# Kernel optimization log

Hardware: AMD Instinct MI355X
Metric: run time of the kernel (lower is better)

## Reference

```python
import jax, jax.numpy as jnp
import numpy as np

CAR_DIM = 8
ESC_MAX_AGENT = 32
HID = 256
ACTION_DIM = 30
NUM_STATES = 64
BATCH = 8192
ENC_OUT = 1 + CAR_DIM * ESC_MAX_AGENT          # 257
Q_IN = 1 + CAR_DIM + CAR_DIM * ESC_MAX_AGENT   # 265


def setup_inputs() -> dict:
    key = jax.random.key(0)
    ks = jax.random.split(key, 9)
    s = jax.random.normal(ks[0], (BATCH, CAR_DIM + NUM_STATES * CAR_DIM), dtype=jnp.float32)
    def lin(k, fan_in, fan_out):
        bound = 1.0 / np.sqrt(fan_in)
        kw, kb = jax.random.split(k)
        W = jax.random.uniform(kw, (fan_in, fan_out), jnp.float32, -bound, bound)
        b = jax.random.uniform(kb, (fan_out,), jnp.float32, -bound, bound)
        return W, b
    W1, b1 = lin(ks[1], CAR_DIM, HID)
    W2, b2 = lin(ks[2], HID, ENC_OUT)
    Qw1, Qb1 = lin(ks[3], Q_IN, HID)
    Qw2, Qb2 = lin(ks[4], HID, ACTION_DIM)
    return {"s": s, "W1": W1, "b1": b1, "W2": W2, "b2": b2,
            "Qw1": Qw1, "Qb1": Qb1, "Qw2": Qw2, "Qb2": Qb2}


def reference(s, W1, b1, W2, b2, Qw1, Qb1, Qw2, Qb2):
    B = s.shape[0]
    self_states = s[:, :CAR_DIM]                                   # [B, C]
    surr = s[:, CAR_DIM:].reshape(B, -1, CAR_DIM)                  # [B, N, C]
    # sentinel agents: any coordinate exactly == -1 is skipped
    valid = ~jnp.any(surr == -1.0, axis=-1)                        # [B, N] bool
    h = jax.nn.relu(jnp.einsum('bnc,ch->bnh', surr, W1) + b1)      # [B, N, HID]
    enc = jax.nn.relu(jnp.einsum('bnh,he->bne', h, W2) + b2)       # [B, N, ENC_OUT]
    sum_outputs = jnp.sum(enc * valid[:, :, None].astype(enc.dtype), axis=1)  # [B, ENC_OUT]
    x = jnp.concatenate([self_states, sum_outputs], axis=1)        # [B, Q_IN]
    q = jax.nn.relu(x @ Qw1 + Qb1) @ Qw2 + Qb2                     # [B, ACTION_DIM]
    return q
```

## Files before the change

kernel.cpp:

```cpp
#include <hip/hip_runtime.h>

#define CAR 8
#define SROW 520
#define HID 256
#define EOUT 257
#define XPAD 288
#define ADIM 30

typedef __attribute__((ext_vector_type(8))) short sh8;
typedef __attribute__((ext_vector_type(4))) float f32x4;

__device__ __forceinline__ short f2bf(float f) {
  unsigned u = __builtin_bit_cast(unsigned, f);
  u += 0x7fffu + ((u >> 16) & 1u);
  return (short)(u >> 16);
}
__device__ __forceinline__ unsigned f2bf2(float a, float b) {
  unsigned ua = __builtin_bit_cast(unsigned, a);
  ua += 0x7fffu + ((ua >> 16) & 1u);
  unsigned ub = __builtin_bit_cast(unsigned, b);
  ub += 0x7fffu + ((ub >> 16) & 1u);
  return __builtin_amdgcn_perm(ub, ua, 0x07060302);
}
__device__ __forceinline__ unsigned pkt(float a, float b) {
  return __builtin_amdgcn_perm(__builtin_bit_cast(unsigned, b),
                               __builtin_bit_cast(unsigned, a), 0x07060302);
}

__global__ void k_prep(const float* __restrict__ W1, const float* __restrict__ b1,
                       const float* __restrict__ W2,
                       const float* __restrict__ Qw1, const float* __restrict__ Qw2,
                       short* __restrict__ w1f, short* __restrict__ w2f,
                       short* __restrict__ w3f, short* __restrict__ wq2f) {
  int idx = blockIdx.x * 256 + threadIdx.x;
  if (idx < 8192) {
    int mt = idx >> 9, r = idx & 511, lane = r >> 3, j = r & 7;
    int quad = lane >> 4, m = lane & 15;
    int hid = mt * 16 + m;
    float v = (quad == 0) ? W1[j * HID + hid]
            : (quad == 1 && j == 0) ? b1[hid] : 0.0f;
    w1f[idx] = f2bf(v);
    return;
  }
  int i2 = idx - 8192;
  if (i2 < 69632) {
    int ks = i2 / 8704, r = i2 % 8704;
    int nt = r >> 9, r2 = r & 511, lane = r2 >> 3, j = r2 & 7;
    int quad = lane >> 4, m = lane & 15;
    int k = ks * 32 + quad * 8 + j, n = nt * 16 + m;
    float v = (n < EOUT) ? W2[k * EOUT + n] : 0.0f;
    w2f[i2] = f2bf(v);
    return;
  }
  int i3 = i2 - 69632;
  if (i3 < 73728) {
    int ks = i3 >> 13, r = i3 & 8191;
    int nt = r >> 9, r2 = r & 511, lane = r2 >> 3, j = r2 & 7;
    int quad = lane >> 4, m = lane & 15;
    int k = ks * 32 + quad * 8 + j, n = nt * 16 + m;
    float v = (k < 265) ? Qw1[k * HID + n] : 0.0f;
    w3f[i3] = f2bf(v);
    return;
  }
  int i4 = i3 - 73728;
  if (i4 < 8192) {
    int ks = i4 >> 10, r = i4 & 1023;
    int nt = r >> 9, r2 = r & 511, lane = r2 >> 3, j = r2 & 7;
    int quad = lane >> 4, m = lane & 15;
    int k = ks * 32 + quad * 8 + j, n = nt * 16 + m;
    float v = (n < ADIM) ? Qw2[k * ADIM + n] : 0.0f;
    wq2f[i4] = f2bf(v);
  }
}

__global__ __launch_bounds__(512, 4)
void k_enc(const float* __restrict__ s, const short* __restrict__ w1f,
           const short* __restrict__ w2f, const float* __restrict__ b2,
           float* __restrict__ so288, int B) {
  __shared__ __align__(16) short hlds[2][16384];
  __shared__ float ninvp[8];
  __shared__ float t16[8][16];

  const int tid = threadIdx.x;
  const int w = tid >> 6, lane = tid & 63;
  const int q = lane >> 4, m = lane & 15;
  const int we = w >> 2, g = w & 3;
  const size_t bg0 = 2 * (size_t)blockIdx.x;
  size_t bg = bg0 + we; if (bg >= (size_t)B) bg = B - 1;

  const float* srow0 = s + bg * SROW + CAR;
  int4 pk = {0, 0, 0, 0};
  bool inv = false;
  if (lane < 16) {
    const float* sr = srow0 + (g * 16 + lane) * CAR;
    float4 f0 = ((const float4*)sr)[0], f1 = ((const float4*)sr)[1];
    inv = (f0.x == -1.f) | (f0.y == -1.f) | (f0.z == -1.f) | (f0.w == -1.f) |
          (f1.x == -1.f) | (f1.y == -1.f) | (f1.z == -1.f) | (f1.w == -1.f);
    if (!inv) {
      pk.x = (int)f2bf2(f0.x, f0.y); pk.y = (int)f2bf2(f0.z, f0.w);
      pk.z = (int)f2bf2(f1.x, f1.y); pk.w = (int)f2bf2(f1.z, f1.w);
    }
  }
  const float vflag = inv ? 0.f : 1.f;
  unsigned long long bal = __ballot(inv);
  if (lane == 0) ninvp[w] = (float)__popcll(bal);

  if (w == 1 || w == 2) {
    size_t rr = bg0 + (w - 1); if (rr >= (size_t)B) rr = B - 1;
    if (lane < CAR)       so288[rr * XPAD + lane] = s[rr * SROW + lane];
    else if (lane < 16)   so288[rr * XPAD + 280 + (lane - 8)] = 0.f;
  }

  int4 p0;
  p0.x = __shfl(pk.x, m, 64); p0.y = __shfl(pk.y, m, 64);
  p0.z = __shfl(pk.z, m, 64); p0.w = __shfl(pk.w, m, 64);
  const float vv0 = __shfl(vflag, m, 64);
  if (q == 1) {
    p0.x = (vv0 != 0.f) ? 0x3f80 : 0; p0.y = p0.z = p0.w = 0;
  } else if (q >= 2) {
    p0.x = p0.y = p0.z = p0.w = 0;
  }
  sh8 bs = __builtin_bit_cast(sh8, p0);

#pragma unroll 4
  for (int mt = 0; mt < 16; ++mt) {
    sh8 af = *(const sh8*)(w1f + (mt * 64 + lane) * 8);
    f32x4 z = {0.f, 0.f, 0.f, 0.f};
    f32x4 c0 = __builtin_amdgcn_mfma_f32_16x16x32_bf16(af, bs, z, 0, 0, 0);
    const int hidb = mt * 16 + q * 4;
    const int ks = hidb >> 5, qB = (hidb >> 3) & 3, js = hidb & 7;
    uint2 k0;
    k0.x = pkt(fmaxf(c0[0], 0.f), fmaxf(c0[1], 0.f));
    k0.y = pkt(fmaxf(c0[2], 0.f), fmaxf(c0[3], 0.f));
    *(uint2*)(&hlds[we][((g * 8 + ks) * 64 + qB * 16 + m) * 8 + js]) = k0;
  }
  __syncthreads();

  const int t0 = 2 * w;
  const float bi0  = b2[t0 * 16 + m];
  const float bi1  = b2[t0 * 16 + 16 + m];
  const float bi16 = (m == 0) ? b2[256] : 0.f;
  f32x4 acc[4][2][2];
  f32x4 acc16 = {bi16, bi16, bi16, bi16};
#pragma unroll
  for (int mtA = 0; mtA < 4; ++mtA)
#pragma unroll
    for (int e = 0; e < 2; ++e) {
      f32x4 c0 = {bi0, bi0, bi0, bi0};
      f32x4 c1 = {bi1, bi1, bi1, bi1};
      acc[mtA][0][e] = c0;
      acc[mtA][1][e] = c1;
    }
#pragma unroll
  for (int ks = 0; ks < 8; ++ks) {
    sh8 B0  = *(const sh8*)(w2f + ((ks * 17 + t0)     * 64 + lane) * 8);
    sh8 B1  = *(const sh8*)(w2f + ((ks * 17 + t0 + 1) * 64 + lane) * 8);
    sh8 B16 = *(const sh8*)(w2f + ((ks * 17 + 16)     * 64 + lane) * 8);
#pragma unroll
    for (int e = 0; e < 2; ++e) {
      sh8 A0 = *(const sh8*)(&hlds[e][(0 * 8 + ks) * 512 + lane * 8]);
      sh8 A1 = *(const sh8*)(&hlds[e][(1 * 8 + ks) * 512 + lane * 8]);
      sh8 A2 = *(const sh8*)(&hlds[e][(2 * 8 + ks) * 512 + lane * 8]);
      sh8 A3 = *(const sh8*)(&hlds[e][(3 * 8 + ks) * 512 + lane * 8]);
      __builtin_amdgcn_s_setprio(1);
      acc[0][0][e] = __builtin_amdgcn_mfma_f32_16x16x32_bf16(A0, B0, acc[0][0][e], 0, 0, 0);
      acc[1][0][e] = __builtin_amdgcn_mfma_f32_16x16x32_bf16(A1, B0, acc[1][0][e], 0, 0, 0);
      acc[2][0][e] = __builtin_amdgcn_mfma_f32_16x16x32_bf16(A2, B0, acc[2][0][e], 0, 0, 0);
      acc[3][0][e] = __builtin_amdgcn_mfma_f32_16x16x32_bf16(A3, B0, acc[3][0][e], 0, 0, 0);
      acc[0][1][e] = __builtin_amdgcn_mfma_f32_16x16x32_bf16(A0, B1, acc[0][1][e], 0, 0, 0);
      acc[1][1][e] = __builtin_amdgcn_mfma_f32_16x16x32_bf16(A1, B1, acc[1][1][e], 0, 0, 0);
      acc[2][1][e] = __builtin_amdgcn_mfma_f32_16x16x32_bf16(A2, B1, acc[2][1][e], 0, 0, 0);
      acc[3][1][e] = __builtin_amdgcn_mfma_f32_16x16x32_bf16(A3, B1, acc[3][1][e], 0, 0, 0);
      if (we == e) {
        if (g == 0)      acc16 = __builtin_amdgcn_mfma_f32_16x16x32_bf16(A0, B16, acc16, 0, 0, 0);
        else if (g == 1) acc16 = __builtin_amdgcn_mfma_f32_16x16x32_bf16(A1, B16, acc16, 0, 0, 0);
        else if (g == 2) acc16 = __builtin_amdgcn_mfma_f32_16x16x32_bf16(A2, B16, acc16, 0, 0, 0);
        else             acc16 = __builtin_amdgcn_mfma_f32_16x16x32_bf16(A3, B16, acc16, 0, 0, 0);
      }
      __builtin_amdgcn_s_setprio(0);
    }
  }

  const float ninv[2] = {ninvp[0] + ninvp[1] + ninvp[2] + ninvp[3],
                         ninvp[4] + ninvp[5] + ninvp[6] + ninvp[7]};
#pragma unroll
  for (int i = 0; i < 2; ++i) {
    const int col = (t0 + i) * 16 + m;
    const float bic = (i == 0) ? bi0 : bi1;
    const float rb2 = fmaxf(bic, 0.f);
#pragma unroll
    for (int e = 0; e < 2; ++e) {
      float ssum = 0.f;
#pragma unroll
      for (int mtA = 0; mtA < 4; ++mtA)
#pragma unroll
        for (int r = 0; r < 4; ++r)
          ssum += fmaxf(acc[mtA][i][e][r], 0.f);
      ssum += __shfl_xor(ssum, 16, 64);
      ssum += __shfl_xor(ssum, 32, 64);
      ssum -= ninv[e] * rb2;
      if (q == 0) {
        size_t rr = bg0 + e; if (rr >= (size_t)B) rr = B - 1;
        so288[rr * XPAD + CAR + col] = ssum;
      }
    }
  }
  {
    float s16 = 0.f;
#pragma unroll
    for (int r = 0; r < 4; ++r)
      s16 += fmaxf(acc16[r], 0.f);
    s16 += __shfl_xor(s16, 16, 64);
    s16 += __shfl_xor(s16, 32, 64);
    if (q == 0) t16[w][m] = s16;
  }
  __syncthreads();
  if ((w == 0 || w == 4) && q == 0) {
    const int e2 = w >> 2;
    const float b2c = (m == 0) ? b2[256] : 0.f;
    const float tot = t16[e2 * 4 + 0][m] + t16[e2 * 4 + 1][m] +
                      t16[e2 * 4 + 2][m] + t16[e2 * 4 + 3][m]
                    - ninv[e2] * fmaxf(b2c, 0.f);
    size_t rr2 = bg0 + e2; if (rr2 >= (size_t)B) rr2 = B - 1;
    so288[rr2 * XPAD + CAR + 256 + m] = tot;
  }
}

__global__ __launch_bounds__(256, 2)
void k_q(const float* __restrict__ so288, const short* __restrict__ w3f,
         const float* __restrict__ Qb1, const short* __restrict__ wq2f,
         const float* __restrict__ Qb2, float* __restrict__ out, int B) {
  __shared__ __align__(16) short xf[9 * 64 * 8];
  __shared__ __align__(16) float H[16 * 260];
  const int tid = threadIdx.x;
  const int w = tid >> 6, lane = tid & 63;
  const int q = lane >> 4, m = lane & 15;
  const int b0 = blockIdx.x * 16;

#pragma unroll
  for (int it = 0; it < 3; ++it) {
    int sidx = tid + it * 256;
    if (sidx < 576) {
      int ks = sidx >> 6, l = sidx & 63;
      int lq = l >> 4, lm = l & 15;
      int row = b0 + lm; if (row >= B) row = B - 1;
      const float* xp = so288 + (size_t)row * XPAD + ks * 32 + lq * 8;
      float4 xa = ((const float4*)xp)[0], xb = ((const float4*)xp)[1];
      int4 t = {(int)f2bf2(xa.x, xa.y), (int)f2bf2(xa.z, xa.w),
                (int)f2bf2(xb.x, xb.y), (int)f2bf2(xb.z, xb.w)};
      *(int4*)(xf + sidx * 8) = t;
    }
  }
  __syncthreads();

  f32x4 acc1[4];
#pragma unroll
  for (int i = 0; i < 4; ++i) {
    f32x4 z = {0.f, 0.f, 0.f, 0.f};
    acc1[i] = z;
  }
#pragma unroll
  for (int ks = 0; ks < 9; ++ks) {
    sh8 A0 = *(const sh8*)(xf + (ks * 64 + lane) * 8);
#pragma unroll
    for (int i = 0; i < 4; ++i) {
      sh8 Bf = *(const sh8*)(w3f + ((ks * 16 + 4 * w + i) * 64 + lane) * 8);
      acc1[i] = __builtin_amdgcn_mfma_f32_16x16x32_bf16(A0, Bf, acc1[i], 0, 0, 0);
    }
  }
#pragma unroll
  for (int i = 0; i < 4; ++i) {
    const int hcol = (4 * w + i) * 16 + m;
    const float bq = Qb1[hcol];
#pragma unroll
    for (int r = 0; r < 4; ++r)
      H[(q * 4 + r) * 260 + hcol] = fmaxf(acc1[i][r] + bq, 0.f);
  }
  __syncthreads();

  if (w < 2) {
    f32x4 acc2 = {0.f, 0.f, 0.f, 0.f};
#pragma unroll
    for (int ks = 0; ks < 8; ++ks) {
      const float* hp = H + m * 260 + ks * 32 + q * 8;
      float4 ha = ((const float4*)hp)[0], hb = ((const float4*)hp)[1];
      int4 t = {(int)f2bf2(ha.x, ha.y), (int)f2bf2(ha.z, ha.w),
                (int)f2bf2(hb.x, hb.y), (int)f2bf2(hb.z, hb.w)};
      sh8 A2 = __builtin_bit_cast(sh8, t);
      sh8 Bf = *(const sh8*)(wq2f + ((ks * 2 + w) * 64 + lane) * 8);
      acc2 = __builtin_amdgcn_mfma_f32_16x16x32_bf16(A2, Bf, acc2, 0, 0, 0);
    }
    const int act = w * 16 + m;
    if (act < ADIM) {
      const float bq = Qb2[act];
#pragma unroll
      for (int r = 0; r < 4; ++r) {
        const int row = b0 + q * 4 + r;
        if (row < B) out[(size_t)row * ADIM + act] = acc2[r] + bq;
      }
    }
  }
}

extern "C" void kernel_launch(void* const* d_in, const int* in_sizes, int n_in,
                              void* d_out, int out_size, void* d_ws, size_t ws_size,
                              hipStream_t stream) {
  const float* s   = (const float*)d_in[0];
  const float* W1  = (const float*)d_in[1];
  const float* b1  = (const float*)d_in[2];
  const float* W2  = (const float*)d_in[3];
  const float* b2  = (const float*)d_in[4];
  const float* Qw1 = (const float*)d_in[5];
  const float* Qb1 = (const float*)d_in[6];
  const float* Qw2 = (const float*)d_in[7];
  const float* Qb2 = (const float*)d_in[8];
  float* out = (float*)d_out;
  const int B = in_sizes[0] / SROW;

  char* wsb = (char*)d_ws;
  float* so288 = (float*)wsb;
  size_t off = (size_t)B * XPAD * sizeof(float);
  short* w1f  = (short*)(wsb + off);            off += 8192 * 2;
  short* w2f  = (short*)(wsb + off);            off += 69632 * 2;
  short* w3f  = (short*)(wsb + off);            off += 73728 * 2;
  short* wq2f = (short*)(wsb + off);

  const int prep_elems = 8192 + 69632 + 73728 + 8192;
  k_prep<<<(prep_elems + 255) / 256, 256, 0, stream>>>(W1, b1, W2, Qw1, Qw2,
                                                       w1f, w2f, w3f, wq2f);
  k_enc<<<(B + 1) / 2, 512, 0, stream>>>(s, w1f, w2f, b2, so288, B);
  k_q<<<(B + 15) / 16, 256, 0, stream>>>(so288, w3f, Qb1, wq2f, Qb2, out, B);
}
```

Before: 162.7 us.

## Split hidden layer into halves to overlap layer-1 compute with layer-2 MFMAs

Splits the LDS buffer for the first-layer activations into two halves. The second half of layer 1 is computed after the first barrier and is interleaved with the layer-2 MFMAs over the first half's K range, followed by a second barrier and the rest of the K range. This is meant to hide layer-1 latency behind layer-2 matrix work. It also drops the s_setprio hints and adds an extra __syncthreads.

```diff
diff --git a/kernel.cpp b/kernel.cpp
--- a/kernel.cpp
+++ b/kernel.cpp
@@ -77,7 +77,8 @@
 void k_enc(const float* __restrict__ s, const short* __restrict__ w1f,
            const short* __restrict__ w2f, const float* __restrict__ b2,
            float* __restrict__ so288, int B) {
-  __shared__ __align__(16) short hlds[2][16384];
+  __shared__ __align__(16) short hldsA[2][8192];
+  __shared__ __align__(16) short hldsB[2][8192];
   __shared__ float ninvp[8];
   __shared__ float t16[8][16];
 
@@ -123,7 +124,7 @@
   sh8 bs = __builtin_bit_cast(sh8, p0);
 
 #pragma unroll 4
-  for (int mt = 0; mt < 16; ++mt) {
+  for (int mt = 0; mt < 8; ++mt) {
     sh8 af = *(const sh8*)(w1f + (mt * 64 + lane) * 8);
     f32x4 z = {0.f, 0.f, 0.f, 0.f};
     f32x4 c0 = __builtin_amdgcn_mfma_f32_16x16x32_bf16(af, bs, z, 0, 0, 0);
@@ -132,7 +133,7 @@
     uint2 k0;
     k0.x = pkt(fmaxf(c0[0], 0.f), fmaxf(c0[1], 0.f));
     k0.y = pkt(fmaxf(c0[2], 0.f), fmaxf(c0[3], 0.f));
-    *(uint2*)(&hlds[we][((g * 8 + ks) * 64 + qB * 16 + m) * 8 + js]) = k0;
+    *(uint2*)(&hldsA[we][((g * 4 + ks) * 64 + qB * 16 + m) * 8 + js]) = k0;
   }
   __syncthreads();
 
@@ -151,18 +152,30 @@
       acc[mtA][0][e] = c0;
       acc[mtA][1][e] = c1;
     }
-#pragma unroll
-  for (int ks = 0; ks < 8; ++ks) {
+
+#pragma unroll 4
+  for (int mt = 8; mt < 16; ++mt) {
+    sh8 af = *(const sh8*)(w1f + (mt * 64 + lane) * 8);
+    f32x4 z = {0.f, 0.f, 0.f, 0.f};
+    f32x4 c0 = __builtin_amdgcn_mfma_f32_16x16x32_bf16(af, bs, z, 0, 0, 0);
+    const int hidb = mt * 16 + q * 4;
+    const int ks2 = (hidb >> 5) - 4, qB = (hidb >> 3) & 3, js = hidb & 7;
+    uint2 k0;
+    k0.x = pkt(fmaxf(c0[0], 0.f), fmaxf(c0[1], 0.f));
+    k0.y = pkt(fmaxf(c0[2], 0.f), fmaxf(c0[3], 0.f));
+    *(uint2*)(&hldsB[we][((g * 4 + ks2) * 64 + qB * 16 + m) * 8 + js]) = k0;
+  }
+#pragma unroll
+  for (int ks = 0; ks < 4; ++ks) {
     sh8 B0  = *(const sh8*)(w2f + ((ks * 17 + t0)     * 64 + lane) * 8);
     sh8 B1  = *(const sh8*)(w2f + ((ks * 17 + t0 + 1) * 64 + lane) * 8);
     sh8 B16 = *(const sh8*)(w2f + ((ks * 17 + 16)     * 64 + lane) * 8);
 #pragma unroll
     for (int e = 0; e < 2; ++e) {
-      sh8 A0 = *(const sh8*)(&hlds[e][(0 * 8 + ks) * 512 + lane * 8]);
-      sh8 A1 = *(const sh8*)(&hlds[e][(1 * 8 + ks) * 512 + lane * 8]);
-      sh8 A2 = *(const sh8*)(&hlds[e][(2 * 8 + ks) * 512 + lane * 8]);
-      sh8 A3 = *(const sh8*)(&hlds[e][(3 * 8 + ks) * 512 + lane * 8]);
-      __builtin_amdgcn_s_setprio(1);
+      sh8 A0 = *(const sh8*)(&hldsA[e][((0 * 4 + ks) * 64 + lane) * 8]);
+      sh8 A1 = *(const sh8*)(&hldsA[e][((1 * 4 + ks) * 64 + lane) * 8]);
+      sh8 A2 = *(const sh8*)(&hldsA[e][((2 * 4 + ks) * 64 + lane) * 8]);
+      sh8 A3 = *(const sh8*)(&hldsA[e][((3 * 4 + ks) * 64 + lane) * 8]);
       acc[0][0][e] = __builtin_amdgcn_mfma_f32_16x16x32_bf16(A0, B0, acc[0][0][e], 0, 0, 0);
       acc[1][0][e] = __builtin_amdgcn_mfma_f32_16x16x32_bf16(A1, B0, acc[1][0][e], 0, 0, 0);
       acc[2][0][e] = __builtin_amdgcn_mfma_f32_16x16x32_bf16(A2, B0, acc[2][0][e], 0, 0, 0);
@@ -177,7 +190,35 @@
         else if (g == 2) acc16 = __builtin_amdgcn_mfma_f32_16x16x32_bf16(A2, B16, acc16, 0, 0, 0);
         else             acc16 = __builtin_amdgcn_mfma_f32_16x16x32_bf16(A3, B16, acc16, 0, 0, 0);
       }
-      __builtin_amdgcn_s_setprio(0);
+    }
+  }
+  __syncthreads();
+
+#pragma unroll
+  for (int ks = 0; ks < 4; ++ks) {
+    sh8 B0  = *(const sh8*)(w2f + (((ks + 4) * 17 + t0)     * 64 + lane) * 8);
+    sh8 B1  = *(const sh8*)(w2f + (((ks + 4) * 17 + t0 + 1) * 64 + lane) * 8);
+    sh8 B16 = *(const sh8*)(w2f + (((ks + 4) * 17 + 16)     * 64 + lane) * 8);
+#pragma unroll
+    for (int e = 0; e < 2; ++e) {
+      sh8 A0 = *(const sh8*)(&hldsB[e][((0 * 4 + ks) * 64 + lane) * 8]);
+      sh8 A1 = *(const sh8*)(&hldsB[e][((1 * 4 + ks) * 64 + lane) * 8]);
+      sh8 A2 = *(const sh8*)(&hldsB[e][((2 * 4 + ks) * 64 + lane) * 8]);
+      sh8 A3 = *(const sh8*)(&hldsB[e][((3 * 4 + ks) * 64 + lane) * 8]);
+      acc[0][0][e] = __builtin_amdgcn_mfma_f32_16x16x32_bf16(A0, B0, acc[0][0][e], 0, 0, 0);
+      acc[1][0][e] = __builtin_amdgcn_mfma_f32_16x16x32_bf16(A1, B0, acc[1][0][e], 0, 0, 0);
+      acc[2][0][e] = __builtin_amdgcn_mfma_f32_16x16x32_bf16(A2, B0, acc[2][0][e], 0, 0, 0);
+      acc[3][0][e] = __builtin_amdgcn_mfma_f32_16x16x32_bf16(A3, B0, acc[3][0][e], 0, 0, 0);
+      acc[0][1][e] = __builtin_amdgcn_mfma_f32_16x16x32_bf16(A0, B1, acc[0][1][e], 0, 0, 0);
+      acc[1][1][e] = __builtin_amdgcn_mfma_f32_16x16x32_bf16(A1, B1, acc[1][1][e], 0, 0, 0);
+      acc[2][1][e] = __builtin_amdgcn_mfma_f32_16x16x32_bf16(A2, B1, acc[2][1][e], 0, 0, 0);
+      acc[3][1][e] = __builtin_amdgcn_mfma_f32_16x16x32_bf16(A3, B1, acc[3][1][e], 0, 0, 0);
+      if (we == e) {
+        if (g == 0)      acc16 = __builtin_amdgcn_mfma_f32_16x16x32_bf16(A0, B16, acc16, 0, 0, 0);
+        else if (g == 1) acc16 = __builtin_amdgcn_mfma_f32_16x16x32_bf16(A1, B16, acc16, 0, 0, 0);
+        else if (g == 2) acc16 = __builtin_amdgcn_mfma_f32_16x16x32_bf16(A2, B16, acc16, 0, 0, 0);
+        else             acc16 = __builtin_amdgcn_mfma_f32_16x16x32_bf16(A3, B16, acc16, 0, 0, 0);
+      }
     }
   }
 
```

Measured after the change: 172.4 us. +6.0%, slower.
